# Optimization experiments

Measured on AMD Instinct MI355X. Metric: run time of the kernel, lower is better.

Reference implementation:

```python
import jax, jax.numpy as jnp
import numpy as np

EMB_DIM = 128
WALK_LEN = 40
WINDOW = 5
NEG_SIZE = 5
NEG_WEIGHT = 1.0
NUM_NODES = 1_000_000
BATCH = 512


def _pair_indices(walk_length=WALK_LEN, window_size=WINDOW):
    # replicates the idx_list_src / idx_list_dst construction in __init__
    src, dst = [], []
    for i in range(walk_length):
        for j in range(max(0, i - window_size), i):
            src.append(j); dst.append(i)
        for j in range(i + 1, min(walk_length, i + 1 + window_size)):
            src.append(j); dst.append(i)
    return np.asarray(src, dtype=np.int64), np.asarray(dst, dtype=np.int64)

_SRC, _DST = _pair_indices()  # each has 370 entries
NUM_PAIRS = _SRC.shape[0]


def setup_inputs() -> dict:
    key = jax.random.key(0)
    k1, k2, k3, k4 = jax.random.split(key, 4)
    batch_walk = jax.random.randint(k1, (BATCH, WALK_LEN), 0, NUM_NODES, dtype=jnp.int64)
    neg_idx_dst = jax.random.randint(k2, (BATCH * NUM_PAIRS * NEG_SIZE,), 0, BATCH * WALK_LEN, dtype=jnp.int64)
    init_range = 1.0 / EMB_DIM
    node_embed = jax.random.normal(k3, (NUM_NODES, EMB_DIM), dtype=jnp.float32) * init_range
    context_embed = jax.random.normal(k4, (NUM_NODES, EMB_DIM), dtype=jnp.float32) * init_range
    return {"batch_walk": batch_walk, "neg_idx_dst": neg_idx_dst,
            "node_embed": node_embed, "context_embed": context_embed}


def reference(batch_walk, neg_idx_dst, node_embed, context_embed):
    B = batch_walk.shape[0]
    flat_walk = batch_walk.reshape(-1)                      # [B*L]
    batch_node = node_embed[flat_walk]                      # [B*L, D]
    batch_ctx = context_embed[flat_walk]                    # [B*L, D]

    offsets = (jnp.arange(B, dtype=jnp.int64) * WALK_LEN)[:, None]
    idx_src = (offsets + jnp.asarray(_SRC)[None, :]).reshape(-1)  # [B*370]
    idx_dst = (offsets + jnp.asarray(_DST)[None, :]).reshape(-1)  # [B*370]

    pos_src = batch_node[idx_src]
    pos_dst = batch_ctx[idx_dst]
    pos_score = jnp.clip(jnp.sum(pos_src * pos_dst, axis=1), -6.0, 6.0)
    pos_loss = jnp.mean(-jax.nn.log_sigmoid(pos_score))

    neg_idx_src = jnp.repeat(idx_dst, NEG_SIZE)             # [B*370*NEG]
    neg_src = batch_node[neg_idx_src]
    neg_dst = batch_ctx[neg_idx_dst]
    neg_score = jnp.clip(jnp.sum(neg_src * neg_dst, axis=1), -6.0, 6.0)
    neg_loss = jnp.mean(-jax.nn.log_sigmoid(-neg_score)) * NEG_SIZE * NEG_WEIGHT

    return pos_loss + neg_loss
```

## Files before the change

### kernel.cpp

```cpp
#include <hip/hip_runtime.h>

#define WALK_LEN 40
#define WINDOW   5
#define NPAIRS   370
#define BATCHSZ  512
#define NEGK     5
#define NPOS     (BATCHSZ * NPAIRS)
#define EMB      128
#define NQ       (BATCHSZ * WALK_LEN)
#define THREADS  512
#define GROUPS   (THREADS / 8)
#define HALFP    185
#define NBLOCKS  (BATCHSZ * 2)

struct PairTab { short src[NPAIRS]; short dst[NPAIRS]; };

constexpr PairTab make_pairs() {
    PairTab t{};
    int k = 0;
    for (int i = 0; i < WALK_LEN; ++i) {
        int lo = (i - WINDOW > 0) ? (i - WINDOW) : 0;
        for (int j = lo; j < i; ++j) { t.src[k] = (short)j; t.dst[k] = (short)i; ++k; }
        int hi = (i + 1 + WINDOW < WALK_LEN) ? (i + 1 + WINDOW) : WALK_LEN;
        for (int j = i + 1; j < hi; ++j) { t.src[k] = (short)j; t.dst[k] = (short)i; ++k; }
    }
    return t;
}

__constant__ PairTab g_pairs = make_pairs();

__device__ __forceinline__ unsigned short bf16rn(float f) {
    unsigned u = __float_as_uint(f);
    u += 0x7fffu + ((u >> 16) & 1u);
    return (unsigned short)(u >> 16);
}

__device__ __forceinline__ float softplus_fast(float x) {
    return __logf(1.0f + __expf(x));
}

template <int CTRL>
__device__ __forceinline__ float dpp_qperm_add(float x) {
    int y = __builtin_amdgcn_update_dpp(0, __float_as_int(x), CTRL, 0xF, 0xF, true);
    return x + __int_as_float(y);
}
__device__ __forceinline__ float grp8_sum(float d) {
    d = dpp_qperm_add<0xB1>(d);
    d = dpp_qperm_add<0x4E>(d);
    int y = __builtin_amdgcn_ds_swizzle(__float_as_int(d), 0x101F);
    return d + __int_as_float(y);
}

#define UNPACK_U4(u, f, base)                                         \
    do {                                                              \
        _Pragma("unroll")                                             \
        for (int _i = 0; _i < 4; ++_i) {                              \
            const unsigned _v = (&(u).x)[_i];                         \
            (f)[(base) + 2 * _i]     = __uint_as_float(_v << 16);     \
            (f)[(base) + 2 * _i + 1] = __uint_as_float(_v & 0xffff0000u); \
        }                                                             \
    } while (0)

__device__ __forceinline__ float dot_pk(const float* nf, uint4 xa, uint4 xb) {
    float s0 = 0.f, s1 = 0.f, s2 = 0.f, s3 = 0.f;
    #pragma unroll
    for (int i = 0; i < 4; ++i) {
        const unsigned v = (&xa.x)[i];
        s0 = fmaf(__uint_as_float(v << 16),          nf[2 * i],     s0);
        s1 = fmaf(__uint_as_float(v & 0xffff0000u),  nf[2 * i + 1], s1);
    }
    #pragma unroll
    for (int i = 0; i < 4; ++i) {
        const unsigned v = (&xb.x)[i];
        s2 = fmaf(__uint_as_float(v << 16),          nf[8 + 2 * i],     s2);
        s3 = fmaf(__uint_as_float(v & 0xffff0000u),  nf[8 + 2 * i + 1], s3);
    }
    return (s0 + s1) + (s2 + s3);
}

__global__ __launch_bounds__(256) void dw_gather(
    const int*   __restrict__ walk,
    const float* __restrict__ nodeE,
    const float* __restrict__ ctxE,
    unsigned short* __restrict__ dN,
    unsigned short* __restrict__ dC,
    float* __restrict__ out)
{
    if (blockIdx.x == 0 && threadIdx.x == 0) out[0] = 0.f;
    int idx = blockIdx.x * 256 + threadIdx.x;
    const int is_ctx = (idx >= NQ * 32);
    if (is_ctx) idx -= NQ * 32;
    const int q = idx >> 5, c = idx & 31;
    const int row = walk[q];
    const float* src = (is_ctx ? ctxE : nodeE) + (size_t)row * EMB;
    const float4 v = *((const float4*)src + c);
    ushort4 o;
    o.x = bf16rn(v.x); o.y = bf16rn(v.y); o.z = bf16rn(v.z); o.w = bf16rn(v.w);
    unsigned short* dst = (is_ctx ? dC : dN) + (size_t)q * EMB;
    *((ushort4*)dst + c) = o;
}

__global__ __launch_bounds__(THREADS) void dw_score(
    const int* __restrict__ negdst,
    const unsigned short* __restrict__ dN,
    const unsigned short* __restrict__ dC,
    float* __restrict__ out)
{
    __shared__ unsigned int sN[WALK_LEN * 64];
    __shared__ unsigned int sC[WALK_LEN * 64];
    __shared__ float wsum[THREADS / 64];

    const int b    = blockIdx.x >> 1;
    const int half = blockIdx.x & 1;
    const int tid  = threadIdx.x;

    {
        const uint4* srcN = (const uint4*)(dN + (size_t)b * WALK_LEN * EMB);
        const uint4* srcC = (const uint4*)(dC + (size_t)b * WALK_LEN * EMB);
        for (int u = tid; u < WALK_LEN * 16; u += THREADS) {
            ((uint4*)sN)[u] = srcN[u];
            ((uint4*)sC)[u] = srcC[u];
        }
    }
    __syncthreads();

    const int lane8 = tid & 7;
    const int grp   = tid >> 3;
    const int jbase = half * HALFP;
    float acc = 0.0f;

    #pragma unroll 1
    for (int it = 0; it < 3; ++it) {
        const int jj = it * GROUPS + grp;
        if (jj < HALFP) {
            const int j = jbase + jj;
            const int p = b * NPAIRS + j;
            const int sj = g_pairs.src[j];
            const int dj = g_pairs.dst[j];

            const int* nb = negdst + p * NEGK;
            const int q0 = nb[0], q1 = nb[1], q2 = nb[2], q3 = nb[3], q4 = nb[4];

            const uint4* g0 = (const uint4*)(dC + (size_t)q0 * EMB);
            const uint4* g1 = (const uint4*)(dC + (size_t)q1 * EMB);
            const uint4* g2 = (const uint4*)(dC + (size_t)q2 * EMB);
            const uint4* g3 = (const uint4*)(dC + (size_t)q3 * EMB);
            const uint4* g4 = (const uint4*)(dC + (size_t)q4 * EMB);
            const uint4 x00 = g0[lane8], x01 = g0[lane8 + 8];
            const uint4 x10 = g1[lane8], x11 = g1[lane8 + 8];
            const uint4 x20 = g2[lane8], x21 = g2[lane8 + 8];
            const uint4 x30 = g3[lane8], x31 = g3[lane8 + 8];
            const uint4 x40 = g4[lane8], x41 = g4[lane8 + 8];

            const uint4* rN = (const uint4*)(sN + sj * 64);
            const uint4* rC = (const uint4*)(sC + dj * 64);
            const uint4* rS = (const uint4*)(sN + dj * 64);
            const uint4 a0 = rN[lane8], a1 = rN[lane8 + 8];
            const uint4 c0 = rC[lane8], c1 = rC[lane8 + 8];
            const uint4 n0 = rS[lane8], n1 = rS[lane8 + 8];

            {
                float af[16];
                UNPACK_U4(a0, af, 0);
                UNPACK_U4(a1, af, 8);
                float d = grp8_sum(dot_pk(af, c0, c1));
                const float s = fminf(6.f, fmaxf(-6.f, d));
                acc += softplus_fast(-s);
            }

            {
                float nf[16];
                UNPACK_U4(n0, nf, 0);
                UNPACK_U4(n1, nf, 8);
                float d0 = grp8_sum(dot_pk(nf, x00, x01));
                float d1 = grp8_sum(dot_pk(nf, x10, x11));
                float d2 = grp8_sum(dot_pk(nf, x20, x21));
                float d3 = grp8_sum(dot_pk(nf, x30, x31));
                float d4 = grp8_sum(dot_pk(nf, x40, x41));
                acc += softplus_fast(fminf(6.f, fmaxf(-6.f, d0)));
                acc += softplus_fast(fminf(6.f, fmaxf(-6.f, d1)));
                acc += softplus_fast(fminf(6.f, fmaxf(-6.f, d2)));
                acc += softplus_fast(fminf(6.f, fmaxf(-6.f, d3)));
                acc += softplus_fast(fminf(6.f, fmaxf(-6.f, d4)));
            }
        }
    }

    acc += __shfl_xor(acc, 8);
    acc += __shfl_xor(acc, 16);
    acc += __shfl_xor(acc, 32);

    if ((tid & 63) == 0) wsum[tid >> 6] = acc;
    __syncthreads();
    if (tid == 0) {
        float tot = 0.f;
        #pragma unroll
        for (int w = 0; w < THREADS / 64; ++w) tot += wsum[w];
        atomicAdd(out, tot * (1.0f / (float)NPOS));
    }
}

extern "C" void kernel_launch(void* const* d_in, const int* in_sizes, int n_in,
                              void* d_out, int out_size, void* d_ws, size_t ws_size,
                              hipStream_t stream) {
    const int*   walk   = (const int*)d_in[0];
    const int*   negdst = (const int*)d_in[1];
    const float* nodeE  = (const float*)d_in[2];
    const float* ctxE   = (const float*)d_in[3];
    float*       out    = (float*)d_out;

    unsigned short* dN = (unsigned short*)d_ws;
    unsigned short* dC = dN + (size_t)NQ * EMB;

    dw_gather<<<(2 * NQ * 32) / 256, 256, 0, stream>>>(walk, nodeE, ctxE, dN, dC, out);
    dw_score<<<NBLOCKS, THREADS, 0, stream>>>(negdst, dN, dC, out);
}
```

Before: 39.03 us.

## Flatten score kernel to one pair per 8-lane group, drop LDS staging

The score kernel no longer stages each walk's node and context rows in shared memory, and it no longer loops three times per block over half a walk's pairs. Each 8-lane group now handles exactly one global pair, reading all rows straight from the bf16 workspace through cache, so the grid grows to NPOS/64 blocks with no stage barrier. The group-of-8 reduction's final step uses a DPP row shift instead of ds_swizzle. The change trades the LDS fill and barrier, plus idle groups in the last iteration, for more global/L2 traffic and more blocks each doing a final atomicAdd.

```diff
diff --git a/kernel.cpp b/kernel.cpp
--- a/kernel.cpp
+++ b/kernel.cpp
@@ -9,9 +9,7 @@
 #define EMB      128
 #define NQ       (BATCHSZ * WALK_LEN)
 #define THREADS  512
-#define GROUPS   (THREADS / 8)
-#define HALFP    185
-#define NBLOCKS  (BATCHSZ * 2)
+#define SBLOCKS  (NPOS / (THREADS / 8))
 
 struct PairTab { short src[NPAIRS]; short dst[NPAIRS]; };
 
@@ -40,15 +38,15 @@
 }
 
 template <int CTRL>
-__device__ __forceinline__ float dpp_qperm_add(float x) {
+__device__ __forceinline__ float dpp_add(float x) {
     int y = __builtin_amdgcn_update_dpp(0, __float_as_int(x), CTRL, 0xF, 0xF, true);
     return x + __int_as_float(y);
 }
 __device__ __forceinline__ float grp8_sum(float d) {
-    d = dpp_qperm_add<0xB1>(d);
-    d = dpp_qperm_add<0x4E>(d);
-    int y = __builtin_amdgcn_ds_swizzle(__float_as_int(d), 0x101F);
-    return d + __int_as_float(y);
+    d = dpp_add<0xB1>(d);
+    d = dpp_add<0x4E>(d);
+    d = dpp_add<0x141>(d);
+    return d;
 }
 
 #define UNPACK_U4(u, f, base)                                         \
@@ -106,90 +104,64 @@
     const unsigned short* __restrict__ dC,
     float* __restrict__ out)
 {
-    __shared__ unsigned int sN[WALK_LEN * 64];
-    __shared__ unsigned int sC[WALK_LEN * 64];
-    __shared__ float wsum[THREADS / 64];
+    const int tid   = threadIdx.x;
+    const int lane8 = tid & 7;
+    const int pid   = (blockIdx.x * THREADS + tid) >> 3;
 
-    const int b    = blockIdx.x >> 1;
-    const int half = blockIdx.x & 1;
-    const int tid  = threadIdx.x;
+    const int b  = pid / NPAIRS;
+    const int j  = pid - b * NPAIRS;
+    const int arow = b * WALK_LEN + g_pairs.src[j];
+    const int drow = b * WALK_LEN + g_pairs.dst[j];
 
+    const int* nb = negdst + pid * NEGK;
+    const int q0 = nb[0], q1 = nb[1], q2 = nb[2], q3 = nb[3], q4 = nb[4];
+
+    const uint4* gA = (const uint4*)(dN + (size_t)arow * EMB);
+    const uint4* gC = (const uint4*)(dC + (size_t)drow * EMB);
+    const uint4* gS = (const uint4*)(dN + (size_t)drow * EMB);
+    const uint4* g0 = (const uint4*)(dC + (size_t)q0 * EMB);
+    const uint4* g1 = (const uint4*)(dC + (size_t)q1 * EMB);
+    const uint4* g2 = (const uint4*)(dC + (size_t)q2 * EMB);
+    const uint4* g3 = (const uint4*)(dC + (size_t)q3 * EMB);
+    const uint4* g4 = (const uint4*)(dC + (size_t)q4 * EMB);
+    const uint4 a0  = gA[lane8], a1  = gA[lane8 + 8];
+    const uint4 c0  = gC[lane8], c1  = gC[lane8 + 8];
+    const uint4 n0  = gS[lane8], n1  = gS[lane8 + 8];
+    const uint4 x00 = g0[lane8], x01 = g0[lane8 + 8];
+    const uint4 x10 = g1[lane8], x11 = g1[lane8 + 8];
+    const uint4 x20 = g2[lane8], x21 = g2[lane8 + 8];
+    const uint4 x30 = g3[lane8], x31 = g3[lane8 + 8];
+    const uint4 x40 = g4[lane8], x41 = g4[lane8 + 8];
+
+    float acc;
     {
-        const uint4* srcN = (const uint4*)(dN + (size_t)b * WALK_LEN * EMB);
-        const uint4* srcC = (const uint4*)(dC + (size_t)b * WALK_LEN * EMB);
-        for (int u = tid; u < WALK_LEN * 16; u += THREADS) {
-            ((uint4*)sN)[u] = srcN[u];
-            ((uint4*)sC)[u] = srcC[u];
-        }
+        float af[16];
+        UNPACK_U4(a0, af, 0);
+        UNPACK_U4(a1, af, 8);
+        const float d = grp8_sum(dot_pk(af, c0, c1));
+        acc = softplus_fast(-fminf(6.f, fmaxf(-6.f, d)));
     }
-    __syncthreads();
-
-    const int lane8 = tid & 7;
-    const int grp   = tid >> 3;
-    const int jbase = half * HALFP;
-    float acc = 0.0f;
-
-    #pragma unroll 1
-    for (int it = 0; it < 3; ++it) {
-        const int jj = it * GROUPS + grp;
-        if (jj < HALFP) {
-            const int j = jbase + jj;
-            const int p = b * NPAIRS + j;
-            const int sj = g_pairs.src[j];
-            const int dj = g_pairs.dst[j];
-
-            const int* nb = negdst + p * NEGK;
-            const int q0 = nb[0], q1 = nb[1], q2 = nb[2], q3 = nb[3], q4 = nb[4];
-
-            const uint4* g0 = (const uint4*)(dC + (size_t)q0 * EMB);
-            const uint4* g1 = (const uint4*)(dC + (size_t)q1 * EMB);
-            const uint4* g2 = (const uint4*)(dC + (size_t)q2 * EMB);
-            const uint4* g3 = (const uint4*)(dC + (size_t)q3 * EMB);
-            const uint4* g4 = (const uint4*)(dC + (size_t)q4 * EMB);
-            const uint4 x00 = g0[lane8], x01 = g0[lane8 + 8];
-            const uint4 x10 = g1[lane8], x11 = g1[lane8 + 8];
-            const uint4 x20 = g2[lane8], x21 = g2[lane8 + 8];
-            const uint4 x30 = g3[lane8], x31 = g3[lane8 + 8];
-            const uint4 x40 = g4[lane8], x41 = g4[lane8 + 8];
-
-            const uint4* rN = (const uint4*)(sN + sj * 64);
-            const uint4* rC = (const uint4*)(sC + dj * 64);
-            const uint4* rS = (const uint4*)(sN + dj * 64);
-            const uint4 a0 = rN[lane8], a1 = rN[lane8 + 8];
-            const uint4 c0 = rC[lane8], c1 = rC[lane8 + 8];
-            const uint4 n0 = rS[lane8], n1 = rS[lane8 + 8];
-
-            {
-                float af[16];
-                UNPACK_U4(a0, af, 0);
-                UNPACK_U4(a1, af, 8);
-                float d = grp8_sum(dot_pk(af, c0, c1));
-                const float s = fminf(6.f, fmaxf(-6.f, d));
-                acc += softplus_fast(-s);
-            }
-
-            {
-                float nf[16];
-                UNPACK_U4(n0, nf, 0);
-                UNPACK_U4(n1, nf, 8);
-                float d0 = grp8_sum(dot_pk(nf, x00, x01));
-                float d1 = grp8_sum(dot_pk(nf, x10, x11));
-                float d2 = grp8_sum(dot_pk(nf, x20, x21));
-                float d3 = grp8_sum(dot_pk(nf, x30, x31));
-                float d4 = grp8_sum(dot_pk(nf, x40, x41));
-                acc += softplus_fast(fminf(6.f, fmaxf(-6.f, d0)));
-                acc += softplus_fast(fminf(6.f, fmaxf(-6.f, d1)));
-                acc += softplus_fast(fminf(6.f, fmaxf(-6.f, d2)));
-                acc += softplus_fast(fminf(6.f, fmaxf(-6.f, d3)));
-                acc += softplus_fast(fminf(6.f, fmaxf(-6.f, d4)));
-            }
-        }
+    {
+        float nf[16];
+        UNPACK_U4(n0, nf, 0);
+        UNPACK_U4(n1, nf, 8);
+        const float d0 = grp8_sum(dot_pk(nf, x00, x01));
+        const float d1 = grp8_sum(dot_pk(nf, x10, x11));
+        const float d2 = grp8_sum(dot_pk(nf, x20, x21));
+        const float d3 = grp8_sum(dot_pk(nf, x30, x31));
+        const float d4 = grp8_sum(dot_pk(nf, x40, x41));
+        acc += softplus_fast(fminf(6.f, fmaxf(-6.f, d0)));
+        acc += softplus_fast(fminf(6.f, fmaxf(-6.f, d1)));
+        acc += softplus_fast(fminf(6.f, fmaxf(-6.f, d2)));
+        acc += softplus_fast(fminf(6.f, fmaxf(-6.f, d3)));
+        acc += softplus_fast(fminf(6.f, fmaxf(-6.f, d4)));
     }
 
     acc += __shfl_xor(acc, 8);
     acc += __shfl_xor(acc, 16);
     acc += __shfl_xor(acc, 32);
 
+    __shared__ float wsum[THREADS / 64];
     if ((tid & 63) == 0) wsum[tid >> 6] = acc;
     __syncthreads();
     if (tid == 0) {
@@ -213,5 +185,5 @@
     unsigned short* dC = dN + (size_t)NQ * EMB;
 
     dw_gather<<<(2 * NQ * 32) / 256, 256, 0, stream>>>(walk, nodeE, ctxE, dN, dC, out);
-    dw_score<<<NBLOCKS, THREADS, 0, stream>>>(negdst, dN, dC, out);
+    dw_score<<<SBLOCKS, THREADS, 0, stream>>>(negdst, dN, dC, out);
 }
```

Result: slower. 57.94 us (+48.5%).
